# Optimization experiments

Measured on AMD Instinct MI355X. Metric: run time of the kernel, lower is better.

## Reference

```python
import jax, jax.numpy as jnp
import numpy as np

N_NODES = 50000
NODE_IN, NODE_OUT, EDGE_IN = 128, 64, 32
N_EDGES = 400000
ALPHA = 0.2  # LeakyReLU negative slope
EPS = 1e-12  # F.normalize clamp


def setup_inputs() -> dict:
    key = jax.random.key(0)
    ks = jax.random.split(key, 6)
    node_fts = jax.random.normal(ks[0], (N_NODES, NODE_IN), dtype=jnp.float32)
    edge_fts = jax.random.normal(ks[1], (N_EDGES, EDGE_IN), dtype=jnp.float32)
    edges = jax.random.randint(ks[2], (2, N_EDGES), 0, N_NODES)
    # W_node: Linear(node_in, node_out); store weight as [in, out] for x @ W
    W = jax.random.normal(ks[3], (NODE_IN, NODE_OUT), dtype=jnp.float32) * (1.414 * (6.0 / (NODE_IN + NODE_OUT)) ** 0.5)
    b = jnp.zeros((NODE_OUT,), dtype=jnp.float32)
    a_node = jax.random.normal(ks[4], (2 * NODE_OUT + EDGE_IN, 1), dtype=jnp.float32) * 0.1
    scale = jnp.ones((), dtype=jnp.float32)  # MessageNorm learned scale
    return {"node_fts": node_fts, "edge_fts": edge_fts, "edges": edges,
            "W": W, "b": b, "a_node": a_node, "scale": scale}


def reference(node_fts, edge_fts, edges, W, b, a_node, scale):
    # edges: [2, E] -> reshape (row-major, as in torch) to [E, 2]
    e = edges.reshape(-1, 2)                                  # [E, 2]
    eu = jnp.concatenate([e, e[:, ::-1]], axis=0)             # undirected [2E, 2]
    ef_u = jnp.concatenate([edge_fts, edge_fts], axis=0)      # [2E, edge_in]
    src, dst = eu[:, 0], eu[:, 1]

    h_v = node_fts @ W + b                                    # [N, out]

    # per-edge attention logits: cat(h_src, h_dst, edge_ft) @ a
    feat = jnp.concatenate([h_v[src], h_v[dst], ef_u], axis=1)  # [2E, 2*out+edge_in]
    att = jnp.exp(jax.nn.leaky_relu(feat @ a_node, negative_slope=ALPHA))  # [2E, 1]

    att_sum = jax.ops.segment_sum(att, src, num_segments=N_NODES)[src]     # [2E, 1]
    att_norm = jnp.log(att / att_sum)                          # log-softmax over dst per src
    att_var = jnp.var(att_norm, ddof=1)                        # torch.var (unbiased)

    msg = jax.ops.segment_sum(h_v[dst] * att_norm, src, num_segments=N_NODES)  # [N, out]

    # MessageNorm(learn_scale=True): l2-normalize msg, rescale by ||h_v|| * scale
    msg_n = msg / jnp.maximum(jnp.linalg.norm(msg, axis=-1, keepdims=True), EPS)
    agg = msg_n * jnp.linalg.norm(h_v, axis=-1, keepdims=True) * scale

    final_embed = jnp.concatenate([h_v, agg], axis=1)          # [N, 2*out]
    return final_embed, att_var
```

## Files before the change

### kernel.cpp

```cpp
#include <hip/hip_runtime.h>

#define N_NODES 50000
#define NIN 128
#define NOUT 64
#define EIN 32
#define N_EDGES 400000
#define N_UNITS (2 * N_EDGES)
#define ALPHA 0.2f
#define CAP 64
#define N_GATHER_BLOCKS 12500

__device__ __forceinline__ int clampi(int x) {
  return min(max(x, 0), N_NODES - 1);
}

__device__ __forceinline__ unsigned bf16_lo(float f) {
  unsigned u = __float_as_uint(f);
  return (u + 0x7FFFu + ((u >> 16) & 1u)) >> 16;
}
__device__ __forceinline__ unsigned bf16_hi(float f) {
  unsigned u = __float_as_uint(f);
  return (u + 0x7FFFu + ((u >> 16) & 1u)) & 0xFFFF0000u;
}

__global__ __launch_bounds__(256) void k_gemm(
    const float* __restrict__ nf, const float* __restrict__ W,
    const float* __restrict__ b, const float* __restrict__ a,
    const float* __restrict__ ef, float* __restrict__ out,
    unsigned short* __restrict__ hb, float* __restrict__ A,
    float* __restrict__ B, float* __restrict__ hn, float* __restrict__ c,
    int* __restrict__ cnt) {
  __shared__ float rows[8][NIN];
  __shared__ float part[4][8][NOUT];
  int t = threadIdx.x;
  int w = t >> 6, j = t & 63;
  float wq[32];
#pragma unroll
  for (int i = 0; i < 32; ++i) wq[i] = W[(size_t)(32 * w + i) * NOUT + j];
  float bj = b[j], a1j = a[j], a2j = a[64 + j];
  for (int base = blockIdx.x * 8; base < N_NODES; base += gridDim.x * 8) {
    {
      const float4* src =
          (const float4*)(nf + (size_t)(base + (t >> 5)) * NIN);
      ((float4*)rows[t >> 5])[t & 31] = src[t & 31];
    }
    __syncthreads();
    float ac[8] = {0.f, 0.f, 0.f, 0.f, 0.f, 0.f, 0.f, 0.f};
#pragma unroll
    for (int q = 0; q < 8; ++q) {
      float4 x[8];
#pragma unroll
      for (int r = 0; r < 8; ++r)
        x[r] = ((const float4*)&rows[r][32 * w])[q];
#pragma unroll
      for (int r = 0; r < 8; ++r) {
        ac[r] = fmaf(x[r].x, wq[4 * q + 0], ac[r]);
        ac[r] = fmaf(x[r].y, wq[4 * q + 1], ac[r]);
        ac[r] = fmaf(x[r].z, wq[4 * q + 2], ac[r]);
        ac[r] = fmaf(x[r].w, wq[4 * q + 3], ac[r]);
      }
    }
#pragma unroll
    for (int r = 0; r < 8; ++r) part[w][r][j] = ac[r];
    __syncthreads();
#pragma unroll
    for (int s = 0; s < 2; ++s) {
      int r = w + 4 * s;
      int v = base + r;
      float acc = bj + ((part[0][r][j] + part[1][r][j]) +
                        (part[2][r][j] + part[3][r][j]));
      out[(size_t)v * 128 + j] = acc;
      hb[(size_t)v * NOUT + j] = (unsigned short)bf16_lo(acc);
      float pa = acc * a1j, pb = acc * a2j, pn = acc * acc;
      for (int o = 32; o > 0; o >>= 1) {
        pa += __shfl_down(pa, o, 64);
        pb += __shfl_down(pb, o, 64);
        pn += __shfl_down(pn, o, 64);
      }
      if (j == 0) { A[v] = pa; B[v] = pb; hn[v] = sqrtf(pn); }
    }
    __syncthreads();
  }
  int stride = gridDim.x * blockDim.x;
  int tid = blockIdx.x * blockDim.x + t;
  float a3[EIN];
#pragma unroll
  for (int q = 0; q < EIN; ++q) a3[q] = a[128 + q];
  for (int i = tid; i < N_EDGES; i += stride) {
    const float4* efp = (const float4*)(ef + (size_t)i * EIN);
    float cc = 0.f;
#pragma unroll
    for (int q = 0; q < 8; ++q) {
      float4 u = efp[q];
      cc += u.x * a3[4 * q + 0] + u.y * a3[4 * q + 1] +
            u.z * a3[4 * q + 2] + u.w * a3[4 * q + 3];
    }
    c[i] = cc;
  }
  for (int i = tid; i < N_NODES; i += stride) cnt[i] = 0;
}

__global__ __launch_bounds__(256) void k_edge1(
    const int* __restrict__ eb, const float* __restrict__ c,
    const float* __restrict__ A, const float* __restrict__ B,
    int* __restrict__ cnt, unsigned* __restrict__ csr) {
  int i = blockIdx.x * blockDim.x + threadIdx.x;
  if (i >= N_EDGES) return;
  int2 sd = ((const int2*)eb)[i];
  int s = clampi(sd.x), d = clampi(sd.y);
  float cc = c[i];
  float zf = A[s] + B[d] + cc;
  float zr = A[d] + B[s] + cc;
  float lf = zf > 0.f ? zf : ALPHA * zf;
  float lr = zr > 0.f ? zr : ALPHA * zr;
  int ps = atomicAdd(&cnt[s], 1);
  if (ps < CAP) csr[(size_t)s * CAP + ps] = bf16_hi(lf) | (unsigned)d;
  int pd = atomicAdd(&cnt[d], 1);
  if (pd < CAP) csr[(size_t)d * CAP + pd] = bf16_hi(lr) | (unsigned)s;
}

__global__ __launch_bounds__(256) void k_gather(
    const uint4* __restrict__ hb4, const float* __restrict__ hn,
    const int* __restrict__ cnt, const unsigned* __restrict__ csr,
    const float* __restrict__ scale_p, float* __restrict__ out,
    double* __restrict__ parts) {
  __shared__ double s1s[4], s2s[4];
  float scale = scale_p[0];
  int t = threadIdx.x;
  int w = t >> 6;
  int l = t & 63;
  int g = l >> 3;
  int p = l & 7;
  int v = blockIdx.x * 4 + w;
  int deg = min(__builtin_amdgcn_readfirstlane(cnt[v]), CAP);
  int k0 = v * CAP;
  int k1 = k0 + deg;
  float mA[8] = {0.f, 0.f, 0.f, 0.f, 0.f, 0.f, 0.f, 0.f};
  float mB[8] = {0.f, 0.f, 0.f, 0.f, 0.f, 0.f, 0.f, 0.f};
  float Se = 0.f, L1 = 0.f, L2 = 0.f;
  unsigned E = csr[k0 + g];
  for (int kb = k0; kb < k1; kb += 8) {
    unsigned C = E;
    if (kb + 8 < k1) E = csr[kb + 8 + g];
    bool valid = (kb + g) < k1;
    int idx = valid ? (int)(C & 0xFFFFu) : v;
    float lk = valid ? __uint_as_float(C & 0xFFFF0000u) : 0.f;
    float vm = valid ? 1.f : 0.f;
    uint4 q = hb4[(size_t)idx * 8 + p];
    float hv[8];
    hv[0] = __uint_as_float(q.x << 16);
    hv[1] = __uint_as_float(q.x & 0xFFFF0000u);
    hv[2] = __uint_as_float(q.y << 16);
    hv[3] = __uint_as_float(q.y & 0xFFFF0000u);
    hv[4] = __uint_as_float(q.z << 16);
    hv[5] = __uint_as_float(q.z & 0xFFFF0000u);
    hv[6] = __uint_as_float(q.w << 16);
    hv[7] = __uint_as_float(q.w & 0xFFFF0000u);
    Se += valid ? __expf(lk) : 0.f;
    L1 += lk;
    L2 += lk * lk;
#pragma unroll
    for (int cc = 0; cc < 8; ++cc) {
      mA[cc] = fmaf(hv[cc], lk, mA[cc]);
      mB[cc] = fmaf(hv[cc], vm, mB[cc]);
    }
  }
  for (int o = 8; o < 64; o <<= 1) {
    Se += __shfl_xor(Se, o, 64);
    L1 += __shfl_xor(L1, o, 64);
    L2 += __shfl_xor(L2, o, 64);
  }
  float logS = (deg > 0) ? logf(Se) : 0.f;
  float mf[8];
#pragma unroll
  for (int cc = 0; cc < 8; ++cc) mf[cc] = mA[cc] - logS * mB[cc];
  for (int o = 8; o < 64; o <<= 1) {
#pragma unroll
    for (int cc = 0; cc < 8; ++cc) mf[cc] += __shfl_xor(mf[cc], o, 64);
  }
  float nr = 0.f;
#pragma unroll
  for (int cc = 0; cc < 8; ++cc) nr += mf[cc] * mf[cc];
  for (int o = 1; o < 8; o <<= 1) nr += __shfl_xor(nr, o, 64);
  nr = sqrtf(nr);
  float fac = hn[v] * scale / fmaxf(nr, 1e-12f);
  if (g == 0) {
    float4 s0 = make_float4(mf[0] * fac, mf[1] * fac, mf[2] * fac, mf[3] * fac);
    float4 s1 = make_float4(mf[4] * fac, mf[5] * fac, mf[6] * fac, mf[7] * fac);
    float* op = out + (size_t)v * 128 + 64 + p * 8;
    ((float4*)op)[0] = s0;
    ((float4*)op)[1] = s1;
  }
  if (l == 0) {
    double dls = (double)logS, dl1 = (double)L1, dl2 = (double)L2;
    double dd = (double)deg;
    s1s[w] = dl1 - dd * dls;
    s2s[w] = dl2 - 2.0 * dls * dl1 + dd * dls * dls;
  }
  __syncthreads();
  if (t == 0) {
    parts[2 * blockIdx.x] = s1s[0] + s1s[1] + s1s[2] + s1s[3];
    parts[2 * blockIdx.x + 1] = s2s[0] + s2s[1] + s2s[2] + s2s[3];
  }
}

__global__ __launch_bounds__(256) void k_var(const double* __restrict__ parts,
                                             float* __restrict__ out) {
  __shared__ double s1[256], s2[256];
  int t = threadIdx.x;
  double a1 = 0.0, a2 = 0.0;
  for (int i = t; i < N_GATHER_BLOCKS; i += 256) {
    a1 += parts[2 * i];
    a2 += parts[2 * i + 1];
  }
  s1[t] = a1;
  s2[t] = a2;
  __syncthreads();
  for (int o = 128; o > 0; o >>= 1) {
    if (t < o) {
      s1[t] += s1[t + o];
      s2[t] += s2[t + o];
    }
    __syncthreads();
  }
  if (t == 0) {
    double M = (double)N_UNITS;
    double var = (s2[0] - s1[0] * s1[0] / M) / (M - 1.0);
    out[(size_t)N_NODES * 128] = (float)var;
  }
}

extern "C" void kernel_launch(void* const* d_in, const int* in_sizes, int n_in,
                              void* d_out, int out_size, void* d_ws,
                              size_t ws_size, hipStream_t stream) {
  const float* nf = (const float*)d_in[0];
  const float* ef = (const float*)d_in[1];
  const int* eb = (const int*)d_in[2];
  const float* W = (const float*)d_in[3];
  const float* b = (const float*)d_in[4];
  const float* a = (const float*)d_in[5];
  const float* scale_p = (const float*)d_in[6];
  float* out = (float*)d_out;

  char* ws = (char*)d_ws;
  unsigned short* hb = (unsigned short*)(ws + 0);
  unsigned* csr = (unsigned*)(ws + 6400000);
  float* A = (float*)(ws + 19200000);
  float* B = (float*)(ws + 19400000);
  float* hn = (float*)(ws + 19600000);
  int* cnt = (int*)(ws + 19800000);
  double* parts = (double*)(ws + 20000000);
  float* c = (float*)(ws + 20200000);


  k_gemm<<<1024, 256, 0, stream>>>(nf, W, b, a, ef, out, hb, A, B, hn, c, cnt);
  k_edge1<<<(N_EDGES + 255) / 256, 256, 0, stream>>>(eb, c, A, B, cnt, csr);
  k_gather<<<N_GATHER_BLOCKS, 256, 0, stream>>>((const uint4*)hb, hn, cnt, csr,
                                                scale_p, out, parts);
  k_var<<<1, 256, 0, stream>>>(parts, out);
}
```

Baseline: 239.0 us.

## Double node tile to 16 rows and overlap epilogue with next tile load

New measurement: 235.4 us. Within noise of the previous version (-1.5%).

```diff
diff --git a/kernel.cpp b/kernel.cpp
--- a/kernel.cpp
+++ b/kernel.cpp
@@ -30,43 +30,79 @@
     unsigned short* __restrict__ hb, float* __restrict__ A,
     float* __restrict__ B, float* __restrict__ hn, float* __restrict__ c,
     int* __restrict__ cnt) {
-  __shared__ float rows[8][NIN];
-  __shared__ float part[4][8][NOUT];
+  __shared__ float rows[16][NIN];
+  __shared__ float part[4][16][NOUT];
   int t = threadIdx.x;
   int w = t >> 6, j = t & 63;
   float wq[32];
 #pragma unroll
   for (int i = 0; i < 32; ++i) wq[i] = W[(size_t)(32 * w + i) * NOUT + j];
   float bj = b[j], a1j = a[j], a2j = a[64 + j];
-  for (int base = blockIdx.x * 8; base < N_NODES; base += gridDim.x * 8) {
-    {
-      const float4* src =
-          (const float4*)(nf + (size_t)(base + (t >> 5)) * NIN);
-      ((float4*)rows[t >> 5])[t & 31] = src[t & 31];
-    }
+  int prev = -1;
+  for (int base = blockIdx.x * 16; base < N_NODES; base += gridDim.x * 16) {
+    const float4* src = (const float4*)(nf + (size_t)base * NIN);
+    float4 s0 = src[t];
+    float4 s1 = src[t + 256];
+    if (prev >= 0) {
+#pragma unroll
+      for (int e = 0; e < 4; ++e) {
+        int r = 4 * w + e;
+        int v = prev + r;
+        float acc = bj + ((part[0][r][j] + part[1][r][j]) +
+                          (part[2][r][j] + part[3][r][j]));
+        out[(size_t)v * 128 + j] = acc;
+        hb[(size_t)v * NOUT + j] = (unsigned short)bf16_lo(acc);
+        float pa = acc * a1j, pb = acc * a2j, pn = acc * acc;
+        for (int o = 32; o > 0; o >>= 1) {
+          pa += __shfl_down(pa, o, 64);
+          pb += __shfl_down(pb, o, 64);
+          pn += __shfl_down(pn, o, 64);
+        }
+        if (j == 0) { A[v] = pa; B[v] = pb; hn[v] = sqrtf(pn); }
+      }
+    }
+    ((float4*)rows)[t] = s0;
+    ((float4*)rows)[t + 256] = s1;
     __syncthreads();
-    float ac[8] = {0.f, 0.f, 0.f, 0.f, 0.f, 0.f, 0.f, 0.f};
+    float ac[16];
+#pragma unroll
+    for (int r = 0; r < 16; ++r) ac[r] = 0.f;
 #pragma unroll
     for (int q = 0; q < 8; ++q) {
-      float4 x[8];
-#pragma unroll
-      for (int r = 0; r < 8; ++r)
-        x[r] = ((const float4*)&rows[r][32 * w])[q];
-#pragma unroll
-      for (int r = 0; r < 8; ++r) {
-        ac[r] = fmaf(x[r].x, wq[4 * q + 0], ac[r]);
-        ac[r] = fmaf(x[r].y, wq[4 * q + 1], ac[r]);
-        ac[r] = fmaf(x[r].z, wq[4 * q + 2], ac[r]);
-        ac[r] = fmaf(x[r].w, wq[4 * q + 3], ac[r]);
+#pragma unroll
+      for (int rc = 0; rc < 16; rc += 4) {
+        float4 x0 = ((const float4*)&rows[rc + 0][32 * w])[q];
+        float4 x1 = ((const float4*)&rows[rc + 1][32 * w])[q];
+        float4 x2 = ((const float4*)&rows[rc + 2][32 * w])[q];
+        float4 x3 = ((const float4*)&rows[rc + 3][32 * w])[q];
+        ac[rc + 0] = fmaf(x0.x, wq[4 * q + 0], ac[rc + 0]);
+        ac[rc + 0] = fmaf(x0.y, wq[4 * q + 1], ac[rc + 0]);
+        ac[rc + 0] = fmaf(x0.z, wq[4 * q + 2], ac[rc + 0]);
+        ac[rc + 0] = fmaf(x0.w, wq[4 * q + 3], ac[rc + 0]);
+        ac[rc + 1] = fmaf(x1.x, wq[4 * q + 0], ac[rc + 1]);
+        ac[rc + 1] = fmaf(x1.y, wq[4 * q + 1], ac[rc + 1]);
+        ac[rc + 1] = fmaf(x1.z, wq[4 * q + 2], ac[rc + 1]);
+        ac[rc + 1] = fmaf(x1.w, wq[4 * q + 3], ac[rc + 1]);
+        ac[rc + 2] = fmaf(x2.x, wq[4 * q + 0], ac[rc + 2]);
+        ac[rc + 2] = fmaf(x2.y, wq[4 * q + 1], ac[rc + 2]);
+        ac[rc + 2] = fmaf(x2.z, wq[4 * q + 2], ac[rc + 2]);
+        ac[rc + 2] = fmaf(x2.w, wq[4 * q + 3], ac[rc + 2]);
+        ac[rc + 3] = fmaf(x3.x, wq[4 * q + 0], ac[rc + 3]);
+        ac[rc + 3] = fmaf(x3.y, wq[4 * q + 1], ac[rc + 3]);
+        ac[rc + 3] = fmaf(x3.z, wq[4 * q + 2], ac[rc + 3]);
+        ac[rc + 3] = fmaf(x3.w, wq[4 * q + 3], ac[rc + 3]);
       }
     }
 #pragma unroll
-    for (int r = 0; r < 8; ++r) part[w][r][j] = ac[r];
+    for (int r = 0; r < 16; ++r) part[w][r][j] = ac[r];
     __syncthreads();
-#pragma unroll
-    for (int s = 0; s < 2; ++s) {
-      int r = w + 4 * s;
-      int v = base + r;
+    prev = base;
+  }
+  if (prev >= 0) {
+#pragma unroll
+    for (int e = 0; e < 4; ++e) {
+      int r = 4 * w + e;
+      int v = prev + r;
       float acc = bj + ((part[0][r][j] + part[1][r][j]) +
                         (part[2][r][j] + part[3][r][j]));
       out[(size_t)v * 128 + j] = acc;
@@ -79,7 +115,6 @@
       }
       if (j == 0) { A[v] = pa; B[v] = pb; hn[v] = sqrtf(pn); }
     }
-    __syncthreads();
   }
   int stride = gridDim.x * blockDim.x;
   int tid = blockIdx.x * blockDim.x + t;
```
